# Kernel tuning notes

Hardware: AMD Instinct MI355X
Metric: run time of the kernel (lower is better)

## Reference

```python
import jax, jax.numpy as jnp
import numpy as np

B, D, N, F, O = 4096, 256, 128, 128, 256


def setup_inputs() -> dict:
    key = jax.random.key(0)
    ks = jax.random.split(key, 6)
    return {
        "x": jax.random.normal(ks[0], (B, D), dtype=jnp.float32),
        "node_weight": jax.random.normal(ks[1], (N, D + F, F), dtype=jnp.float32),  # torch.randn init
        "node_bias": jax.random.normal(ks[2], (N, F), dtype=jnp.float32),
        "attention": jax.random.normal(ks[3], (N, N), dtype=jnp.float32),
        "out_w": jax.random.normal(ks[4], (F, O), dtype=jnp.float32) * 0.05,  # Linear weight (transposed conv.)
        "out_b": jax.random.normal(ks[5], (O,), dtype=jnp.float32) * 0.05,
        "num_iterations": 3,
    }


def reference(x, node_weight, node_bias, attention, out_w, out_b, num_iterations):
    # connections[i, j] = softmax over j of attention row i
    conn = jax.nn.softmax(attention, axis=1)  # [N, N]
    # Split per-node weight: first F rows act on aggregated states, last D rows on x.
    W_s = node_weight[:, :F, :]   # [N, F, F]
    W_x = node_weight[:, F:, :]   # [N, D, F]
    # x contribution is identical every iteration; precompute once.
    xW = jnp.einsum('bd,ndf->nbf', x, W_x) + node_bias[:, None, :]  # [N, B, F]

    states0 = jnp.zeros((N, B, F), dtype=x.dtype)

    def step(states, _):
        agg = jnp.einsum('ij,jbf->ibf', conn, states)            # attention-weighted aggregation
        new = jax.nn.relu(jnp.einsum('nbf,nfg->nbg', agg, W_s) + xW)
        return new, None

    states, _ = jax.lax.scan(step, states0, None, length=num_iterations)
    final_state = states.mean(axis=0)                            # [B, F]
    return final_state @ out_w + out_b                           # [B, O]
```

## Files before the change

kernel.cpp:

```cpp
#include <hip/hip_runtime.h>

#define DEV __device__ __forceinline__

typedef __attribute__((ext_vector_type(8))) short short8;
typedef __attribute__((ext_vector_type(4))) float floatx4;
typedef __attribute__((ext_vector_type(4))) unsigned short ushort4v;
typedef __attribute__((ext_vector_type(8))) unsigned short ushort8v;

#define Bz 4096
#define Dz 256
#define Nz 128
#define Fz 128
#define Oz 256

static constexpr size_t OFF_CONN = 0;
static constexpr size_t OFF_WT   = 65536;
static constexpr size_t SZ_WT    = (size_t)Nz * 128 * 384 * 2;
static constexpr size_t OFF_OWT  = OFF_WT + SZ_WT;
static constexpr size_t OFF_XB   = OFF_OWT + 65536;
static constexpr size_t OFF_FIN  = OFF_XB + (size_t)Bz * Dz * 2;
static constexpr size_t OFF_ST   = OFF_FIN + (size_t)Bz * Fz * 2;

DEV unsigned short f2bf(float x) {
    unsigned u = __float_as_uint(x);
    u = (u + 0x7FFFu + ((u >> 16) & 1u)) >> 16;
    return (unsigned short)u;
}
DEV float bf2f(unsigned short h) {
    return __uint_as_float(((unsigned)h) << 16);
}

typedef const __attribute__((address_space(1))) void cglobal_void;
typedef __attribute__((address_space(3))) void lds_void;

DEV void gld_lds16(const void* g, void* l) {
    __builtin_amdgcn_global_load_lds((cglobal_void*)g, (lds_void*)l, 16, 0, 0);
}

__global__ __launch_bounds__(64) void k_softmax(const float* __restrict__ att,
                                                unsigned short* __restrict__ conn) {
    int i = blockIdx.x, t = threadIdx.x;
    float a0 = att[i * 128 + t];
    float a1 = att[i * 128 + 64 + t];
    float m = fmaxf(a0, a1);
    for (int o = 32; o > 0; o >>= 1) m = fmaxf(m, __shfl_down(m, o));
    m = __shfl(m, 0);
    float e0 = __expf(a0 - m), e1 = __expf(a1 - m);
    float s = e0 + e1;
    for (int o = 32; o > 0; o >>= 1) s += __shfl_down(s, o);
    s = __shfl(s, 0);
    float inv = 1.f / s;
    conn[i * 128 + t] = f2bf(e0 * inv);
    conn[i * 128 + 64 + t] = f2bf(e1 * inv);
}

__global__ __launch_bounds__(256) void k_transpose(const float* __restrict__ src,
                                                   unsigned short* __restrict__ dst,
                                                   int R, int C, int tilesC,
                                                   long sBatch, long dBatch) {
    __shared__ float ld[32][36];
    int tiles = (R / 32) * tilesC;
    int batch = blockIdx.x / tiles;
    int rem = blockIdx.x % tiles;
    int rt = rem / tilesC, ct = rem % tilesC;
    int t = threadIdx.x;
    int kr = t >> 3, c4 = (t & 7) * 4;
    float4 v = *(const float4*)&src[(size_t)batch * sBatch + (size_t)(rt * 32 + kr) * C + ct * 32 + c4];
    ld[kr][c4 + 0] = v.x; ld[kr][c4 + 1] = v.y; ld[kr][c4 + 2] = v.z; ld[kr][c4 + 3] = v.w;
    __syncthreads();
    int cr = kr, k4 = c4;
    ushort4v o;
    o[0] = f2bf(ld[k4 + 0][cr]);
    o[1] = f2bf(ld[k4 + 1][cr]);
    o[2] = f2bf(ld[k4 + 2][cr]);
    o[3] = f2bf(ld[k4 + 3][cr]);
    *(ushort4v*)&dst[(size_t)batch * dBatch + (size_t)(ct * 32 + cr) * R + rt * 32 + k4] = o;
}

__global__ __launch_bounds__(256) void k_convert(const float* __restrict__ src,
                                                 unsigned short* __restrict__ dst) {
    size_t idx = ((size_t)blockIdx.x * 256 + threadIdx.x) * 4;
    float4 v = *(const float4*)&src[idx];
    ushort4v o;
    o[0] = f2bf(v.x); o[1] = f2bf(v.y); o[2] = f2bf(v.z); o[3] = f2bf(v.w);
    *(ushort4v*)&dst[idx] = o;
}

__global__ __launch_bounds__(256) void k2_agg(const unsigned short* __restrict__ conn,
                                              unsigned short* __restrict__ ST) {
    __shared__ unsigned short lA[128 * 136];
    __shared__ unsigned short lB[2][32 * 128];
    int b = blockIdx.x;
    int t = threadIdx.x, wid = t >> 6, lane = t & 63, q = lane >> 4, cc = lane & 15;
    int wm = (wid >> 1) << 6, wn = (wid & 1) << 6;

#pragma unroll
    for (int it = 0; it < 8; it++) {
        int g = it * 256 + t;
        int row = g >> 4, cg = g & 15;
        *(short8*)&lA[row * 136 + cg * 8] = *(const short8*)&conn[row * 128 + cg * 8];
    }
    floatx4 acc[4][4];
#pragma unroll
    for (int mt = 0; mt < 4; mt++)
#pragma unroll
        for (int nt = 0; nt < 4; nt++) acc[mt][nt] = (floatx4){0.f, 0.f, 0.f, 0.f};

    auto STG = [&](int bufi, int kt) {
#pragma unroll
        for (int it = 0; it < 2; it++) {
            int g = it * 256 + t;
            int j = g >> 4, fg = g & 15;
            int lofs = __builtin_amdgcn_readfirstlane((it * 256 + (wid << 6)) * 8);
            gld_lds16(ST + ((size_t)(kt * 32 + j) * Bz + b) * Fz + fg * 8, &lB[bufi][0] + lofs);
        }
    };
    STG(0, 0);
    STG(1, 1);

#pragma unroll
    for (int kt = 0; kt < 4; kt++) {
        int cur = kt & 1;
        if (kt < 3) asm volatile("s_waitcnt vmcnt(2) lgkmcnt(0)" ::: "memory");
        else        asm volatile("s_waitcnt vmcnt(0) lgkmcnt(0)" ::: "memory");
        __builtin_amdgcn_s_barrier();
        __builtin_amdgcn_sched_barrier(0);
        short8 af[4];
#pragma unroll
        for (int mt = 0; mt < 4; mt++)
            af[mt] = *(const short8*)&lA[(wm + mt * 16 + cc) * 136 + kt * 32 + q * 8];
        short8 bf[4];
#pragma unroll
        for (int nt = 0; nt < 4; nt++) {
            short8 v;
#pragma unroll
            for (int e = 0; e < 8; e++)
                v[e] = (short)lB[cur][(q * 8 + e) * 128 + wn + nt * 16 + cc];
            bf[nt] = v;
        }
#pragma unroll
        for (int mt = 0; mt < 4; mt++)
#pragma unroll
            for (int nt = 0; nt < 4; nt++)
                acc[mt][nt] = __builtin_amdgcn_mfma_f32_16x16x32_bf16(af[mt], bf[nt], acc[mt][nt], 0, 0, 0);
        __builtin_amdgcn_sched_barrier(0);
        __builtin_amdgcn_s_barrier();
        if (kt + 2 < 4) STG(cur, kt + 2);
    }

#pragma unroll
    for (int mt = 0; mt < 4; mt++)
#pragma unroll
        for (int nt = 0; nt < 4; nt++) {
            int f = wn + nt * 16 + cc;
#pragma unroll
            for (int r = 0; r < 4; r++) {
                int il = wm + mt * 16 + q * 4 + r;
                lA[il * 128 + (f ^ ((il & 7) << 3))] = f2bf(acc[mt][nt][r]);
            }
        }
    __syncthreads();
#pragma unroll
    for (int it = 0; it < 8; it++) {
        int idx = it * 256 + t;
        int il = idx >> 4, ch = idx & 15;
        int sch = ch ^ (il & 7);
        ushort8v v = *(const ushort8v*)&lA[il * 128 + sch * 8];
        *(ushort8v*)&ST[((size_t)il * Bz + b) * Fz + ch * 8] = v;
    }
}

template <int KT0>
__global__ __launch_bounds__(256) void k3_fused(unsigned short* __restrict__ ST,
                                                const unsigned short* __restrict__ XB,
                                                const unsigned short* __restrict__ WT,
                                                const float* __restrict__ nb) {
    __shared__ unsigned short lds[3][2][128 * 32];
    int n = blockIdx.x >> 5, bt = blockIdx.x & 31;
    int t = threadIdx.x, wid = t >> 6, lane = t & 63, q = lane >> 4, cc = lane & 15;
    int wm = (wid >> 1) << 6, wn = (wid & 1) << 6;

    const unsigned short* Sg = ST + ((size_t)n * Bz + bt * 128) * Fz;
    const unsigned short* Xg = XB + (size_t)bt * 128 * Dz;
    const unsigned short* Bg = WT + (size_t)n * 128 * 384;

    floatx4 acc[4][4];
#pragma unroll
    for (int mt = 0; mt < 4; mt++)
#pragma unroll
        for (int nt = 0; nt < 4; nt++) acc[mt][nt] = (floatx4){0.f, 0.f, 0.f, 0.f};

    auto STAGE = [&](int bufi, int kt) {
#pragma unroll
        for (int it = 0; it < 2; it++) {
            int g = it * 256 + t;
            int row = g >> 2, kg = g & 3;
            int lofs = __builtin_amdgcn_readfirstlane((it * 256 + (wid << 6)) * 8);
            if (kt < 4)
                gld_lds16(Sg + (size_t)row * Fz + kt * 32 + kg * 8, &lds[bufi][0][0] + lofs);
            else
                gld_lds16(Xg + (size_t)row * Dz + (kt - 4) * 32 + kg * 8, &lds[bufi][0][0] + lofs);
            gld_lds16(Bg + (size_t)row * 384 + kt * 32 + kg * 8, &lds[bufi][1][0] + lofs);
        }
    };
    STAGE(0, KT0);
    STAGE(1, KT0 + 1);
    STAGE(2, KT0 + 2);

#pragma unroll
    for (int kt = KT0; kt < 12; kt++) {
        int cur = (kt - KT0) % 3;
        if (kt < 10)      asm volatile("s_waitcnt vmcnt(8) lgkmcnt(0)" ::: "memory");
        else if (kt < 11) asm volatile("s_waitcnt vmcnt(4) lgkmcnt(0)" ::: "memory");
        else              asm volatile("s_waitcnt vmcnt(0) lgkmcnt(0)" ::: "memory");
        __builtin_amdgcn_s_barrier();
        __builtin_amdgcn_sched_barrier(0);
        short8 af[4], bfr[4];
#pragma unroll
        for (int mt = 0; mt < 4; mt++)
            af[mt] = *(const short8*)&lds[cur][0][(wm + mt * 16 + cc) * 32 + q * 8];
#pragma unroll
        for (int nt = 0; nt < 4; nt++)
            bfr[nt] = *(const short8*)&lds[cur][1][(wn + nt * 16 + cc) * 32 + q * 8];
#pragma unroll
        for (int mt = 0; mt < 4; mt++)
#pragma unroll
            for (int nt = 0; nt < 4; nt++)
                acc[mt][nt] = __builtin_amdgcn_mfma_f32_16x16x32_bf16(af[mt], bfr[nt], acc[mt][nt], 0, 0, 0);
        __builtin_amdgcn_sched_barrier(0);
        __builtin_amdgcn_s_barrier();
        if (kt + 3 < 12) STAGE(cur, kt + 3);
    }

    unsigned short* outT = &lds[0][0][0];
#pragma unroll
    for (int nt = 0; nt < 4; nt++) {
        int f = wn + nt * 16 + cc;
        float bias = nb[n * Fz + f];
#pragma unroll
        for (int mt = 0; mt < 4; mt++) {
#pragma unroll
            for (int r = 0; r < 4; r++) {
                int bl = wm + mt * 16 + q * 4 + r;
                float v = acc[mt][nt][r] + bias;
                outT[bl * 128 + (f ^ ((bl & 7) << 3))] = f2bf(v > 0.f ? v : 0.f);
            }
        }
    }
    __syncthreads();
    size_t base = ((size_t)n * Bz + (size_t)bt * 128) * Fz;
#pragma unroll
    for (int it = 0; it < 8; it++) {
        int idx = it * 256 + t;
        int bl = idx >> 4, ch = idx & 15;
        int sch = ch ^ (bl & 7);
        ushort8v v = *(const ushort8v*)&outT[bl * 128 + sch * 8];
        *(ushort8v*)&ST[base + (size_t)idx * 8] = v;
    }
}

__global__ __launch_bounds__(256) void k4_mean(const unsigned short* __restrict__ S,
                                               unsigned short* __restrict__ fin) {
    int t = threadIdx.x;
    size_t base = (size_t)blockIdx.x * 2048 + (size_t)t * 8;
    float a[8] = {0.f, 0.f, 0.f, 0.f, 0.f, 0.f, 0.f, 0.f};
    for (int n = 0; n < Nz; n++) {
        ushort8v v = *(const ushort8v*)&S[(size_t)n * Bz * Fz + base];
#pragma unroll
        for (int e = 0; e < 8; e++) a[e] += bf2f(v[e]);
    }
    ushort8v o;
#pragma unroll
    for (int e = 0; e < 8; e++) o[e] = f2bf(a[e] * (1.f / 128.f));
    *(ushort8v*)&fin[base] = o;
}

__global__ __launch_bounds__(256) void k5_out(const unsigned short* __restrict__ fin,
                                              const unsigned short* __restrict__ owt,
                                              const float* __restrict__ ob,
                                              float* __restrict__ out) {
    __shared__ unsigned short lA[128 * 32];
    __shared__ unsigned short lB[128 * 32];
    int bt = blockIdx.x >> 1, ct = blockIdx.x & 1;
    int t = threadIdx.x, wid = t >> 6, lane = t & 63, q = lane >> 4, cc = lane & 15;
    int wm = (wid >> 1) << 6, wn = (wid & 1) << 6;

    const unsigned short* Ag = fin + (size_t)bt * 128 * Fz;
    const unsigned short* Bg = owt + (size_t)ct * 128 * Fz;

    floatx4 acc[4][4];
#pragma unroll
    for (int mt = 0; mt < 4; mt++)
#pragma unroll
        for (int nt = 0; nt < 4; nt++) acc[mt][nt] = (floatx4){0.f, 0.f, 0.f, 0.f};

    for (int kt = 0; kt < 4; kt++) {
#pragma unroll
        for (int it = 0; it < 2; it++) {
            int g = it * 256 + t;
            int row = g >> 2, kg = g & 3;
            int lofs = __builtin_amdgcn_readfirstlane((it * 256 + (wid << 6)) * 8);
            gld_lds16(Ag + (size_t)row * Fz + kt * 32 + kg * 8, lA + lofs);
            gld_lds16(Bg + (size_t)row * Fz + kt * 32 + kg * 8, lB + lofs);
        }
        __syncthreads();
        short8 af[4], bfr[4];
#pragma unroll
        for (int mt = 0; mt < 4; mt++)
            af[mt] = *(const short8*)&lA[(wm + mt * 16 + cc) * 32 + q * 8];
#pragma unroll
        for (int nt = 0; nt < 4; nt++)
            bfr[nt] = *(const short8*)&lB[(wn + nt * 16 + cc) * 32 + q * 8];
#pragma unroll
        for (int mt = 0; mt < 4; mt++)
#pragma unroll
            for (int nt = 0; nt < 4; nt++)
                acc[mt][nt] = __builtin_amdgcn_mfma_f32_16x16x32_bf16(af[mt], bfr[nt], acc[mt][nt], 0, 0, 0);
        __syncthreads();
    }
#pragma unroll
    for (int nt = 0; nt < 4; nt++) {
        int o = ct * 128 + wn + nt * 16 + cc;
        float bias = ob[o];
#pragma unroll
        for (int mt = 0; mt < 4; mt++) {
#pragma unroll
            for (int r = 0; r < 4; r++) {
                int b = bt * 128 + wm + mt * 16 + q * 4 + r;
                out[(size_t)b * Oz + o] = acc[mt][nt][r] + bias;
            }
        }
    }
}

extern "C" void kernel_launch(void* const* d_in, const int* in_sizes, int n_in,
                              void* d_out, int out_size, void* d_ws, size_t ws_size,
                              hipStream_t stream) {
    const float* x = (const float*)d_in[0];
    const float* nw = (const float*)d_in[1];
    const float* nb = (const float*)d_in[2];
    const float* att = (const float*)d_in[3];
    const float* ow = (const float*)d_in[4];
    const float* ob = (const float*)d_in[5];
    char* ws = (char*)d_ws;
    unsigned short* CONN = (unsigned short*)(ws + OFF_CONN);
    unsigned short* WT = (unsigned short*)(ws + OFF_WT);
    unsigned short* OWT = (unsigned short*)(ws + OFF_OWT);
    unsigned short* XB = (unsigned short*)(ws + OFF_XB);
    unsigned short* FIN = (unsigned short*)(ws + OFF_FIN);
    unsigned short* ST = (unsigned short*)(ws + OFF_ST);
    float* out = (float*)d_out;

    k_softmax<<<Nz, 64, 0, stream>>>(att, CONN);
    k_transpose<<<Nz * 48, 256, 0, stream>>>(nw, WT, 384, 128, 4, (long)384 * 128, (long)128 * 384);
    k_transpose<<<32, 256, 0, stream>>>(ow, OWT, 128, 256, 8, 0, 0);
    k_convert<<<(Bz * Dz) / 1024, 256, 0, stream>>>(x, XB);

    k3_fused<4><<<Nz * 32, 256, 0, stream>>>(ST, XB, WT, nb);

    for (int it = 0; it < 2; it++) {
        k2_agg<<<Bz, 256, 0, stream>>>(CONN, ST);
        k3_fused<0><<<Nz * 32, 256, 0, stream>>>(ST, XB, WT, nb);
    }

    k4_mean<<<(Bz * Fz) / 2048, 256, 0, stream>>>(ST, FIN);
    k5_out<<<64, 256, 0, stream>>>(FIN, OWT, ob, out);
}
```

Measured before the change: 404.0 us.

## Transpose states into LDS via registers in aggregation kernel for vector B-fragment reads

The aggregation kernel stops using direct global-to-LDS loads and instead loads state tiles into registers, then writes them transposed into a padded LDS buffer. The MFMA B fragments can then be read with one 16-byte LDS load per tile instead of eight scalar 2-byte reads. Loads are prefetched two k-steps ahead in registers with a single barrier per step. The mean kernel also gets its reduction loop unrolled by 8 to expose more loads in flight. The cost is more VGPRs and scalar 2-byte LDS writes during the transpose, with possible bank conflicts at stride 34.

```diff
diff --git a/kernel.cpp b/kernel.cpp
--- a/kernel.cpp
+++ b/kernel.cpp
@@ -89,10 +89,28 @@
 __global__ __launch_bounds__(256) void k2_agg(const unsigned short* __restrict__ conn,
                                               unsigned short* __restrict__ ST) {
     __shared__ unsigned short lA[128 * 136];
-    __shared__ unsigned short lB[2][32 * 128];
+    __shared__ unsigned short lBT[2][128 * 34];
     int b = blockIdx.x;
     int t = threadIdx.x, wid = t >> 6, lane = t & 63, q = lane >> 4, cc = lane & 15;
     int wm = (wid >> 1) << 6, wn = (wid & 1) << 6;
+
+    int j0 = t >> 4, fg0 = t & 15;
+    int j1 = (256 + t) >> 4, fg1 = t & 15;
+
+    ushort8v R[4][2];
+    auto LD = [&](int kt, ushort8v* dst) {
+        dst[0] = *(const ushort8v*)(ST + ((size_t)(kt * 32 + j0) * Bz + b) * Fz + fg0 * 8);
+        dst[1] = *(const ushort8v*)(ST + ((size_t)(kt * 32 + j1) * Bz + b) * Fz + fg1 * 8);
+    };
+    auto WR = [&](const ushort8v* src, unsigned short* buf) {
+#pragma unroll
+        for (int e = 0; e < 8; e++) buf[(fg0 * 8 + e) * 34 + j0] = src[0][e];
+#pragma unroll
+        for (int e = 0; e < 8; e++) buf[(fg1 * 8 + e) * 34 + j1] = src[1][e];
+    };
+
+    LD(0, R[0]);
+    LD(1, R[1]);
 
 #pragma unroll
     for (int it = 0; it < 8; it++) {
@@ -100,52 +118,41 @@
         int row = g >> 4, cg = g & 15;
         *(short8*)&lA[row * 136 + cg * 8] = *(const short8*)&conn[row * 128 + cg * 8];
     }
+
     floatx4 acc[4][4];
 #pragma unroll
     for (int mt = 0; mt < 4; mt++)
 #pragma unroll
         for (int nt = 0; nt < 4; nt++) acc[mt][nt] = (floatx4){0.f, 0.f, 0.f, 0.f};
 
-    auto STG = [&](int bufi, int kt) {
-#pragma unroll
-        for (int it = 0; it < 2; it++) {
-            int g = it * 256 + t;
-            int j = g >> 4, fg = g & 15;
-            int lofs = __builtin_amdgcn_readfirstlane((it * 256 + (wid << 6)) * 8);
-            gld_lds16(ST + ((size_t)(kt * 32 + j) * Bz + b) * Fz + fg * 8, &lB[bufi][0] + lofs);
-        }
-    };
-    STG(0, 0);
-    STG(1, 1);
+    WR(R[0], &lBT[0][0]);
+    LD(2, R[2]);
+    asm volatile("s_waitcnt lgkmcnt(0)" ::: "memory");
+    __builtin_amdgcn_s_barrier();
+    __builtin_amdgcn_sched_barrier(0);
 
 #pragma unroll
     for (int kt = 0; kt < 4; kt++) {
         int cur = kt & 1;
-        if (kt < 3) asm volatile("s_waitcnt vmcnt(2) lgkmcnt(0)" ::: "memory");
-        else        asm volatile("s_waitcnt vmcnt(0) lgkmcnt(0)" ::: "memory");
+        short8 af[4], bfr[4];
+#pragma unroll
+        for (int mt = 0; mt < 4; mt++)
+            af[mt] = *(const short8*)&lA[(wm + mt * 16 + cc) * 136 + kt * 32 + q * 8];
+#pragma unroll
+        for (int nt = 0; nt < 4; nt++)
+            bfr[nt] = *(const short8*)&lBT[cur][(wn + nt * 16 + cc) * 34 + q * 8];
+#pragma unroll
+        for (int mt = 0; mt < 4; mt++)
+#pragma unroll
+            for (int nt = 0; nt < 4; nt++)
+                acc[mt][nt] = __builtin_amdgcn_mfma_f32_16x16x32_bf16(af[mt], bfr[nt], acc[mt][nt], 0, 0, 0);
+        if (kt + 1 < 4) {
+            WR(R[kt + 1], &lBT[cur ^ 1][0]);
+            if (kt + 3 < 4) LD(kt + 3, R[kt + 3]);
+        }
+        asm volatile("s_waitcnt lgkmcnt(0)" ::: "memory");
         __builtin_amdgcn_s_barrier();
         __builtin_amdgcn_sched_barrier(0);
-        short8 af[4];
-#pragma unroll
-        for (int mt = 0; mt < 4; mt++)
-            af[mt] = *(const short8*)&lA[(wm + mt * 16 + cc) * 136 + kt * 32 + q * 8];
-        short8 bf[4];
-#pragma unroll
-        for (int nt = 0; nt < 4; nt++) {
-            short8 v;
-#pragma unroll
-            for (int e = 0; e < 8; e++)
-                v[e] = (short)lB[cur][(q * 8 + e) * 128 + wn + nt * 16 + cc];
-            bf[nt] = v;
-        }
-#pragma unroll
-        for (int mt = 0; mt < 4; mt++)
-#pragma unroll
-            for (int nt = 0; nt < 4; nt++)
-                acc[mt][nt] = __builtin_amdgcn_mfma_f32_16x16x32_bf16(af[mt], bf[nt], acc[mt][nt], 0, 0, 0);
-        __builtin_amdgcn_sched_barrier(0);
-        __builtin_amdgcn_s_barrier();
-        if (kt + 2 < 4) STG(cur, kt + 2);
     }
 
 #pragma unroll
@@ -264,6 +271,7 @@
     int t = threadIdx.x;
     size_t base = (size_t)blockIdx.x * 2048 + (size_t)t * 8;
     float a[8] = {0.f, 0.f, 0.f, 0.f, 0.f, 0.f, 0.f, 0.f};
+#pragma unroll 8
     for (int n = 0; n < Nz; n++) {
         ushort8v v = *(const ushort8v*)&S[(size_t)n * Bz * Fz + base];
 #pragma unroll
```

After: 399.4 us. About the same (-1.1%).
